# Performance work log

Hardware: AMD Instinct MI355X
Metric: run time of the kernel (lower is better)

The kernel has to match this reference:

```python
import jax, jax.numpy as jnp
import numpy as np

B, N, K, D = 4, 2048, 32, 256
TOKEN_DIM = 256
EGO_DIM = 256
NUM_HEADS = 4
LN_EPS = 1e-6


def masked_softmax(logits, mask, axis):
    mask = mask.astype(jnp.bool_)
    while mask.ndim < logits.ndim:
        mask = mask[..., None]
    neg_big = jnp.finfo(logits.dtype).min
    has_any = jnp.any(mask, axis=axis, keepdims=True)
    masked_logits = jnp.where(mask, logits, neg_big)
    masked_logits = jnp.where(has_any, masked_logits, 0.0)
    weights = jax.nn.softmax(masked_logits, axis=axis)
    weights = jnp.where(mask, weights, 0.0)
    denom = jnp.sum(weights, axis=axis, keepdims=True)
    weights = jnp.where(denom > 0, weights / denom, 0.0)
    return weights


def setup_inputs() -> dict:
    key = jax.random.key(0)
    ks = jax.random.split(key, 10)
    inv_tok = jax.random.normal(ks[0], (B, N, K, D), dtype=jnp.float32)
    ego_ctx = jax.random.normal(ks[1], (B, N, EGO_DIM), dtype=jnp.float32)
    r = jax.random.normal(ks[2], (B, N, K, 3), dtype=jnp.float32)
    u = jax.random.normal(ks[3], (B, N, K, 3), dtype=jnp.float32)
    mask = jax.random.randint(ks[4], (B, N, K), 0, 2).astype(jnp.bool_)
    # params
    W_ego = jax.random.normal(ks[5], (EGO_DIM, TOKEN_DIM), dtype=jnp.float32) * 0.05
    b_ego = jnp.zeros((TOKEN_DIM,), dtype=jnp.float32)
    ln_scale = jnp.ones((D,), dtype=jnp.float32)
    ln_bias = jnp.zeros((D,), dtype=jnp.float32)
    W_h = jax.random.normal(ks[6], (D + TOKEN_DIM, TOKEN_DIM), dtype=jnp.float32) * 0.05
    b_h = jnp.zeros((TOKEN_DIM,), dtype=jnp.float32)
    W_logit = jax.random.normal(ks[7], (TOKEN_DIM, NUM_HEADS), dtype=jnp.float32) * 0.01
    b_logit = jnp.zeros((NUM_HEADS,), dtype=jnp.float32)
    return {"inv_tok": inv_tok, "ego_ctx": ego_ctx, "r": r, "u": u, "mask": mask,
            "W_ego": W_ego, "b_ego": b_ego, "ln_scale": ln_scale, "ln_bias": ln_bias,
            "W_h": W_h, "b_h": b_h, "W_logit": W_logit, "b_logit": b_logit}


def reference(inv_tok, ego_ctx, r, u, mask, W_ego, b_ego, ln_scale, ln_bias, W_h, b_h, W_logit, b_logit):
    # ego context projection, broadcast over K
    ego_h = ego_ctx @ W_ego + b_ego                      # (B,N,T)
    ego_b = jnp.broadcast_to(ego_h[:, :, None, :], (B, N, K, TOKEN_DIM))
    # LayerNorm over last axis of inv_tok
    mean = jnp.mean(inv_tok, axis=-1, keepdims=True)
    var = jnp.var(inv_tok, axis=-1, keepdims=True)
    ln = (inv_tok - mean) * jax.lax.rsqrt(var + LN_EPS) * ln_scale + ln_bias
    h = jnp.concatenate([ln, ego_b], axis=-1)            # (B,N,K,D+T)
    h = jax.nn.gelu(h @ W_h + b_h, approximate=True)     # (B,N,K,T)
    logits = h @ W_logit + b_logit                       # (B,N,K,H)
    alpha = masked_softmax(logits, mask, axis=-2)        # (B,N,K,H)
    v_r = jnp.einsum('bnkh,bnkd->bnhd', alpha, r).reshape(B, N, 3 * NUM_HEADS)
    v_u = jnp.einsum('bnkh,bnkd->bnhd', alpha, u).reshape(B, N, 3 * NUM_HEADS)
    return (v_r, v_u, alpha)
```

## Files before the change

kernel.cpp:

```cpp
#include <hip/hip_runtime.h>

typedef float f32x4 __attribute__((ext_vector_type(4)));
typedef short bf16x8 __attribute__((ext_vector_type(8)));

__device__ __forceinline__ unsigned short f2bf(float f){
    unsigned int u = __builtin_bit_cast(unsigned int, f);
    u = u + 0x7fffu + ((u >> 16) & 1u);
    return (unsigned short)(u >> 16);
}
__device__ __forceinline__ float bf2f(unsigned short h){
    unsigned int u = ((unsigned int)h) << 16;
    return __builtin_bit_cast(float, u);
}
__device__ __forceinline__ unsigned int pk2(float a, float b){
    return (unsigned int)f2bf(a) | ((unsigned int)f2bf(b) << 16);
}
__device__ __forceinline__ float gelu_f(float x){
    float t = x * x;
    float u = fmaf(0.044715f, t, 1.0f);
    float y = 1.5957691216057308f * x * u;
    float e = __expf(-y);
    return x * __builtin_amdgcn_rcpf(1.0f + e);
}

__device__ __forceinline__ int packpos(int k, int n, int NT){
    int kt = k >> 5, quad = (k >> 3) & 3, j = k & 7;
    int nt = n >> 4, nl = n & 15;
    return ((kt * NT + nt) * 64 + quad * 16 + nl) * 8 + j;
}

__global__ __launch_bounds__(256) void prep(const float* __restrict__ Wh,
        const float* __restrict__ Wlogit, const float* __restrict__ Wego,
        const float* __restrict__ b_ego, const float* __restrict__ b_h,
        const float* __restrict__ ln_s, const float* __restrict__ ln_b,
        unsigned short* __restrict__ Bp1, unsigned short* __restrict__ BpL,
        unsigned short* __restrict__ Bpc, float* __restrict__ b_combo,
        float* __restrict__ v1){
    __shared__ float rowbuf[256];
    int bid = blockIdx.x, tid = threadIdx.x;
    if (bid < 64){
        int base = (bid * 256 + tid) * 4;
        int k = base >> 8;
        float sc = ln_s[k];
        for (int e = base; e < base + 4; ++e){
            int n = e & 255;
            Bp1[packpos(k, n, 16)] = f2bf(sc * Wh[k * 256 + n]);
        }
    } else if (bid == 64){
        for (int e = tid * 16; e < tid * 16 + 16; ++e){
            int k = e >> 4, n = e & 15;
            float v = (n < 4) ? Wlogit[k * 4 + n] : 0.0f;
            BpL[packpos(k, n, 1)] = f2bf(v);
        }
    } else if (bid == 65){
        float acc = b_h[tid];
        for (int j = 0; j < 256; ++j) acc += b_ego[j] * Wh[(256 + j) * 256 + tid];
        for (int k = 0; k < 256; ++k) acc += ln_b[k] * Wh[k * 256 + tid];
        b_combo[tid] = acc;
    } else if (bid == 66){
        float acc = 0.f;
        for (int k = 0; k < 256; ++k)
            acc += bf2f(f2bf(ln_s[k] * Wh[k * 256 + tid]));
        v1[tid] = acc;
    } else {
        int k = bid - 67;
        rowbuf[tid] = Wego[k * 256 + tid];
        __syncthreads();
        float acc = 0.f;
        const float4* row4 = (const float4*)rowbuf;
        for (int j4 = 0; j4 < 64; ++j4){
            float4 e = row4[j4];
            int j = j4 * 4;
            acc += e.x * Wh[(256 + j) * 256 + tid];
            acc += e.y * Wh[(257 + j) * 256 + tid];
            acc += e.z * Wh[(258 + j) * 256 + tid];
            acc += e.w * Wh[(259 + j) * 256 + tid];
        }
        Bpc[packpos(k, tid, 16)] = f2bf(acc);
    }
}

__global__ __launch_bounds__(256) void ego_gemm(const float* __restrict__ ego_ctx,
        const unsigned short* __restrict__ Bpc, const float* __restrict__ b_combo,
        unsigned short* __restrict__ ego_term){
    const int tid = threadIdx.x, w = tid >> 6, l = tid & 63;
    const int m0 = blockIdx.x * 16;
    const int row = m0 + (l & 15);
    const int kq = (l >> 4) << 3;
    f32x4 acc[4];
    #pragma unroll
    for (int j = 0; j < 4; ++j) acc[j] = 0;
    #pragma unroll
    for (int kt = 0; kt < 8; ++kt){
        const float* ap = ego_ctx + row * 256 + kt * 32 + kq;
        float4 x0 = *(const float4*)ap;
        float4 x1 = *(const float4*)(ap + 4);
        uint4 pu = {pk2(x0.x, x0.y), pk2(x0.z, x0.w), pk2(x1.x, x1.y), pk2(x1.z, x1.w)};
        bf16x8 a = __builtin_bit_cast(bf16x8, pu);
        #pragma unroll
        for (int j = 0; j < 4; ++j){
            int nt = w * 4 + j;
            bf16x8 b = *(const bf16x8*)&Bpc[((kt * 16 + nt) * 64 + l) * 8];
            acc[j] = __builtin_amdgcn_mfma_f32_16x16x32_bf16(a, b, acc[j], 0, 0, 0);
        }
    }
    const int rq = (l >> 4) << 2, colc = l & 15;
    #pragma unroll
    for (int j = 0; j < 4; ++j){
        int n = (w * 4 + j) * 16 + colc;
        float bc = b_combo[n];
        #pragma unroll
        for (int rg = 0; rg < 4; ++rg)
            ego_term[(m0 + rq + rg) * 256 + n] = f2bf(acc[j][rg] + bc);
    }
}

__global__ __launch_bounds__(256) void main_fused(const float* __restrict__ inv,
        const float* __restrict__ rin, const float* __restrict__ uin,
        const int* __restrict__ mask, const float* __restrict__ b_logit,
        const unsigned short* __restrict__ Bp1, const unsigned short* __restrict__ BpL,
        const unsigned short* __restrict__ ego_term, const float* __restrict__ v1g,
        float* __restrict__ out){

    __shared__ unsigned short Albs[64 * 264];
    __shared__ float2 stats_s[64];
    __shared__ float logit_s[256];
    __shared__ float alpha_s[256];

    const int tid = threadIdx.x;
    const int w = tid >> 6, l = tid & 63;
    const int T0 = blockIdx.x * 64;
    const int bn0 = blockIdx.x * 2;
    const int col = l & 15;
    const int kq = (l >> 4) << 3;

    {
        const int r0 = w * 16;
        const float* base = inv + (T0 + r0) * 256 + l * 4;
        #pragma unroll
        for (int rr = 0; rr < 16; ++rr){
            float4 c = *(const float4*)(base + rr * 256);
            uint2 p;
            p.x = pk2(c.x, c.y);
            p.y = pk2(c.z, c.w);
            *(uint2*)&Albs[(r0 + rr) * 264 + l * 4] = p;
        }
    }
    float v1r[4], egv[2][4];
    #pragma unroll
    for (int i = 0; i < 4; ++i){
        int n = w * 64 + i * 16 + col;
        v1r[i]    = v1g[n];
        egv[0][i] = bf2f(ego_term[(bn0    ) * 256 + n]);
        egv[1][i] = bf2f(ego_term[(bn0 + 1) * 256 + n]);
    }
    __syncthreads();

    f32x4 acc[4][4];
    #pragma unroll
    for (int a = 0; a < 4; ++a)
        #pragma unroll
        for (int b = 0; b < 4; ++b) acc[a][b] = 0;
    f32x4 gacc = 0, sacc = 0;
    bf16x8 ones;
    #pragma unroll
    for (int j = 0; j < 8; ++j) ones[j] = (short)0x3F80;

    #pragma unroll
    for (int kt = 0; kt < 8; ++kt){
        const int ko = kt * 32 + kq;
        bf16x8 af[4], bv[4];
        #pragma unroll
        for (int mt = 0; mt < 4; ++mt)
            af[mt] = *(const bf16x8*)&Albs[(mt * 16 + col) * 264 + ko];
        #pragma unroll
        for (int i = 0; i < 4; ++i)
            bv[i] = *(const bf16x8*)&Bp1[((kt * 16 + (w * 4 + i)) * 64 + l) * 8];
        #pragma unroll
        for (int mt = 0; mt < 4; ++mt){
            if (mt == w){
                gacc = __builtin_amdgcn_mfma_f32_16x16x32_bf16(af[mt], af[mt], gacc, 0, 0, 0);
                sacc = __builtin_amdgcn_mfma_f32_16x16x32_bf16(af[mt], ones,   sacc, 0, 0, 0);
            }
            #pragma unroll
            for (int i = 0; i < 4; ++i)
                acc[mt][i] = __builtin_amdgcn_mfma_f32_16x16x32_bf16(af[mt], bv[i], acc[mt][i], 0, 0, 0);
        }
    }
    if ((col >> 2) == (l >> 4)){
        int rg = col & 3;
        float mean = sacc[rg] * (1.0f / 256.0f);
        float var  = gacc[rg] * (1.0f / 256.0f) - mean * mean;
        float rstd = rsqrtf(var + 1e-6f);
        stats_s[w * 16 + col] = float2{rstd, rstd * mean};
    }
    __syncthreads();

    {
        const int rq = (l >> 4) << 2;
        #pragma unroll
        for (int mt = 0; mt < 4; ++mt){
            const int g = mt >> 1;
            float2 st[4];
            #pragma unroll
            for (int rg = 0; rg < 4; ++rg) st[rg] = stats_s[mt * 16 + rq + rg];
            #pragma unroll
            for (int i = 0; i < 4; ++i){
                const int n = w * 64 + i * 16 + col;
                const float base_t = egv[g][i];
                #pragma unroll
                for (int rg = 0; rg < 4; ++rg){
                    float x = fmaf(st[rg].x, acc[mt][i][rg],
                                   fmaf(-st[rg].y, v1r[i], base_t));
                    Albs[(mt * 16 + rq + rg) * 264 + n] = f2bf(gelu_f(x));
                }
            }
        }
    }
    __syncthreads();

    {
        f32x4 lacc = 0;
        #pragma unroll
        for (int kt = 0; kt < 8; ++kt){
            bf16x8 a = *(const bf16x8*)&Albs[(w * 16 + col) * 264 + kt * 32 + kq];
            bf16x8 b = *(const bf16x8*)&BpL[(kt * 64 + l) * 8];
            lacc = __builtin_amdgcn_mfma_f32_16x16x32_bf16(a, b, lacc, 0, 0, 0);
        }
        if (col < 4){
            float bl = b_logit[col];
            const int rq = (l >> 4) << 2;
            #pragma unroll
            for (int rg = 0; rg < 4; ++rg)
                logit_s[(w * 16 + rq + rg) * 4 + col] = lacc[rg] + bl;
        }
    }
    __syncthreads();

    {
        int g = w >> 1;
        int h = ((w & 1) << 1) + (l >> 5);
        int k = l & 31;
        int valid = mask[T0 + g * 32 + k] != 0;
        float lg = logit_s[(g * 32 + k) * 4 + h];
        float val = valid ? lg : -3.0e38f;
        float mx = val;
        #pragma unroll
        for (int off = 16; off >= 1; off >>= 1)
            mx = fmaxf(mx, __shfl_xor(mx, off));
        float e = valid ? __expf(lg - mx) : 0.0f;
        float ssum = e;
        #pragma unroll
        for (int off = 16; off >= 1; off >>= 1)
            ssum += __shfl_xor(ssum, off);
        float a = (ssum > 0.f) ? e / ssum : 0.0f;
        alpha_s[(g * 32 + k) * 4 + h] = a;
        out[196608 + (T0 + g * 32 + k) * 4 + h] = a;
    }
    __syncthreads();

    if (tid < 48){
        int g = tid / 24, rem = tid % 24;
        int which = rem / 12, hd = rem % 12;
        int h = hd / 3, d = hd % 3;
        const float* src = which ? uin : rin;
        const float* sp = src + (T0 + g * 32) * 3 + d;
        float acc2 = 0.f;
        #pragma unroll
        for (int k = 0; k < 32; ++k)
            acc2 += alpha_s[(g * 32 + k) * 4 + h] * sp[k * 3];
        out[which * 98304 + (bn0 + g) * 12 + hd] = acc2;
    }
}

extern "C" void kernel_launch(void* const* d_in, const int* in_sizes, int n_in,
                              void* d_out, int out_size, void* d_ws, size_t ws_size,
                              hipStream_t stream){
    const float* inv    = (const float*)d_in[0];
    const float* ego    = (const float*)d_in[1];
    const float* rin    = (const float*)d_in[2];
    const float* uin    = (const float*)d_in[3];
    const int*   mask   = (const int*)  d_in[4];
    const float* Wego   = (const float*)d_in[5];
    const float* b_ego  = (const float*)d_in[6];
    const float* ln_s   = (const float*)d_in[7];
    const float* ln_b   = (const float*)d_in[8];
    const float* Wh     = (const float*)d_in[9];
    const float* b_h    = (const float*)d_in[10];
    const float* Wlogit = (const float*)d_in[11];
    const float* b_lg   = (const float*)d_in[12];
    float* out = (float*)d_out;

    unsigned short* wsu = (unsigned short*)d_ws;
    unsigned short* Bp1 = wsu;
    unsigned short* Bpc = wsu + 65536;
    unsigned short* BpL = wsu + 131072;
    float* b_combo      = (float*)(wsu + 135168);
    float* v1           = (float*)(wsu + 135680);
    unsigned short* ego_term = wsu + 136192;

    prep<<<323, 256, 0, stream>>>(Wh, Wlogit, Wego, b_ego, b_h, ln_s, ln_b,
                                  Bp1, BpL, Bpc, b_combo, v1);
    ego_gemm<<<512, 256, 0, stream>>>(ego, Bpc, b_combo, ego_term);
    main_fused<<<4096, 256, 0, stream>>>(inv, rin, uin, mask, b_lg,
                                         Bp1, BpL, ego_term, v1, out);
}
```

Measured before the change: 455.7 us.

## Split main GEMM by rows per wave, drop barriers, fuse softmax reduction

Measured after the change: 506.3 us. 1.11x slower.

```diff
diff --git a/kernel.cpp b/kernel.cpp
--- a/kernel.cpp
+++ b/kernel.cpp
@@ -12,8 +12,13 @@
     unsigned int u = ((unsigned int)h) << 16;
     return __builtin_bit_cast(float, u);
 }
-__device__ __forceinline__ unsigned int pk2(float a, float b){
-    return (unsigned int)f2bf(a) | ((unsigned int)f2bf(b) << 16);
+__device__ __forceinline__ unsigned int pk2_rtz(float a, float b){
+    unsigned int ua = __builtin_bit_cast(unsigned int, a);
+    unsigned int ub = __builtin_bit_cast(unsigned int, b);
+    return (ua >> 16) | (ub & 0xffff0000u);
+}
+__device__ __forceinline__ unsigned short bfrtz(float a){
+    return (unsigned short)(__builtin_bit_cast(unsigned int, a) >> 16);
 }
 __device__ __forceinline__ float gelu_f(float x){
     float t = x * x;
@@ -36,7 +41,7 @@
         unsigned short* __restrict__ Bp1, unsigned short* __restrict__ BpL,
         unsigned short* __restrict__ Bpc, float* __restrict__ b_combo,
         float* __restrict__ v1){
-    __shared__ float rowbuf[256];
+    __shared__ float rowbuf[512];
     int bid = blockIdx.x, tid = threadIdx.x;
     if (bid < 64){
         int base = (bid * 256 + tid) * 4;
@@ -53,14 +58,19 @@
             BpL[packpos(k, n, 1)] = f2bf(v);
         }
     } else if (bid == 65){
+        rowbuf[tid]       = b_ego[tid];
+        rowbuf[256 + tid] = ln_b[tid];
+        __syncthreads();
         float acc = b_h[tid];
-        for (int j = 0; j < 256; ++j) acc += b_ego[j] * Wh[(256 + j) * 256 + tid];
-        for (int k = 0; k < 256; ++k) acc += ln_b[k] * Wh[k * 256 + tid];
+        for (int j = 0; j < 256; ++j) acc += rowbuf[j] * Wh[(256 + j) * 256 + tid];
+        for (int k = 0; k < 256; ++k) acc += rowbuf[256 + k] * Wh[k * 256 + tid];
         b_combo[tid] = acc;
     } else if (bid == 66){
+        rowbuf[tid] = ln_s[tid];
+        __syncthreads();
         float acc = 0.f;
         for (int k = 0; k < 256; ++k)
-            acc += bf2f(f2bf(ln_s[k] * Wh[k * 256 + tid]));
+            acc += bf2f(f2bf(rowbuf[k] * Wh[k * 256 + tid]));
         v1[tid] = acc;
     } else {
         int k = bid - 67;
@@ -95,8 +105,12 @@
         const float* ap = ego_ctx + row * 256 + kt * 32 + kq;
         float4 x0 = *(const float4*)ap;
         float4 x1 = *(const float4*)(ap + 4);
-        uint4 pu = {pk2(x0.x, x0.y), pk2(x0.z, x0.w), pk2(x1.x, x1.y), pk2(x1.z, x1.w)};
-        bf16x8 a = __builtin_bit_cast(bf16x8, pu);
+        unsigned int ua[4];
+        ua[0] = ((unsigned int)f2bf(x0.x)) | ((unsigned int)f2bf(x0.y) << 16);
+        ua[1] = ((unsigned int)f2bf(x0.z)) | ((unsigned int)f2bf(x0.w) << 16);
+        ua[2] = ((unsigned int)f2bf(x1.x)) | ((unsigned int)f2bf(x1.y) << 16);
+        ua[3] = ((unsigned int)f2bf(x1.z)) | ((unsigned int)f2bf(x1.w) << 16);
+        bf16x8 a = __builtin_bit_cast(bf16x8, *(uint4*)ua);
         #pragma unroll
         for (int j = 0; j < 4; ++j){
             int nt = w * 4 + j;
@@ -125,42 +139,40 @@
     __shared__ unsigned short Albs[64 * 264];
     __shared__ float2 stats_s[64];
     __shared__ float logit_s[256];
-    __shared__ float alpha_s[256];
 
     const int tid = threadIdx.x;
     const int w = tid >> 6, l = tid & 63;
     const int T0 = blockIdx.x * 64;
     const int bn0 = blockIdx.x * 2;
-    const int col = l & 15;
-    const int kq = (l >> 4) << 3;
+    const int col = l & 15, quad = l >> 4, kq = quad << 3;
+    const int r0 = w * 16;
+    const int gw = w >> 1;
+
+    const int h_sm = ((w & 1) << 1) + (l >> 5);
+    const int k_sm = l & 31;
+    const int row_sm = gw * 32 + k_sm;
+    const int mvalid = mask[T0 + row_sm];
+    const float blg = b_logit[h_sm];
+    const float* rp = rin + (T0 + row_sm) * 3;
+    const float* up = uin + (T0 + row_sm) * 3;
+    float rv0 = rp[0], rv1 = rp[1], rv2 = rp[2];
+    float uv0 = up[0], uv1 = up[1], uv2 = up[2];
 
     {
-        const int r0 = w * 16;
         const float* base = inv + (T0 + r0) * 256 + l * 4;
         #pragma unroll
         for (int rr = 0; rr < 16; ++rr){
             float4 c = *(const float4*)(base + rr * 256);
             uint2 p;
-            p.x = pk2(c.x, c.y);
-            p.y = pk2(c.z, c.w);
+            p.x = pk2_rtz(c.x, c.y);
+            p.y = pk2_rtz(c.z, c.w);
             *(uint2*)&Albs[(r0 + rr) * 264 + l * 4] = p;
         }
     }
-    float v1r[4], egv[2][4];
-    #pragma unroll
-    for (int i = 0; i < 4; ++i){
-        int n = w * 64 + i * 16 + col;
-        v1r[i]    = v1g[n];
-        egv[0][i] = bf2f(ego_term[(bn0    ) * 256 + n]);
-        egv[1][i] = bf2f(ego_term[(bn0 + 1) * 256 + n]);
-    }
-    __syncthreads();
-
-    f32x4 acc[4][4];
-    #pragma unroll
-    for (int a = 0; a < 4; ++a)
-        #pragma unroll
-        for (int b = 0; b < 4; ++b) acc[a][b] = 0;
+
+    f32x4 acc[16];
+    #pragma unroll
+    for (int i = 0; i < 16; ++i) acc[i] = 0;
     f32x4 gacc = 0, sacc = 0;
     bf16x8 ones;
     #pragma unroll
@@ -168,108 +180,91 @@
 
     #pragma unroll
     for (int kt = 0; kt < 8; ++kt){
-        const int ko = kt * 32 + kq;
-        bf16x8 af[4], bv[4];
-        #pragma unroll
-        for (int mt = 0; mt < 4; ++mt)
-            af[mt] = *(const bf16x8*)&Albs[(mt * 16 + col) * 264 + ko];
-        #pragma unroll
-        for (int i = 0; i < 4; ++i)
-            bv[i] = *(const bf16x8*)&Bp1[((kt * 16 + (w * 4 + i)) * 64 + l) * 8];
-        #pragma unroll
-        for (int mt = 0; mt < 4; ++mt){
-            if (mt == w){
-                gacc = __builtin_amdgcn_mfma_f32_16x16x32_bf16(af[mt], af[mt], gacc, 0, 0, 0);
-                sacc = __builtin_amdgcn_mfma_f32_16x16x32_bf16(af[mt], ones,   sacc, 0, 0, 0);
-            }
-            #pragma unroll
-            for (int i = 0; i < 4; ++i)
-                acc[mt][i] = __builtin_amdgcn_mfma_f32_16x16x32_bf16(af[mt], bv[i], acc[mt][i], 0, 0, 0);
-        }
-    }
-    if ((col >> 2) == (l >> 4)){
+        bf16x8 af = *(const bf16x8*)&Albs[(r0 + col) * 264 + kt * 32 + kq];
+        gacc = __builtin_amdgcn_mfma_f32_16x16x32_bf16(af, af,   gacc, 0, 0, 0);
+        sacc = __builtin_amdgcn_mfma_f32_16x16x32_bf16(af, ones, sacc, 0, 0, 0);
+        #pragma unroll
+        for (int nt = 0; nt < 16; ++nt){
+            bf16x8 bv = *(const bf16x8*)&Bp1[((kt * 16 + nt) * 64 + l) * 8];
+            acc[nt] = __builtin_amdgcn_mfma_f32_16x16x32_bf16(af, bv, acc[nt], 0, 0, 0);
+        }
+    }
+
+    if ((col >> 2) == quad){
         int rg = col & 3;
         float mean = sacc[rg] * (1.0f / 256.0f);
         float var  = gacc[rg] * (1.0f / 256.0f) - mean * mean;
         float rstd = rsqrtf(var + 1e-6f);
-        stats_s[w * 16 + col] = float2{rstd, rstd * mean};
-    }
-    __syncthreads();
-
-    {
-        const int rq = (l >> 4) << 2;
-        #pragma unroll
-        for (int mt = 0; mt < 4; ++mt){
-            const int g = mt >> 1;
-            float2 st[4];
-            #pragma unroll
-            for (int rg = 0; rg < 4; ++rg) st[rg] = stats_s[mt * 16 + rq + rg];
-            #pragma unroll
-            for (int i = 0; i < 4; ++i){
-                const int n = w * 64 + i * 16 + col;
-                const float base_t = egv[g][i];
-                #pragma unroll
-                for (int rg = 0; rg < 4; ++rg){
-                    float x = fmaf(st[rg].x, acc[mt][i][rg],
-                                   fmaf(-st[rg].y, v1r[i], base_t));
-                    Albs[(mt * 16 + rq + rg) * 264 + n] = f2bf(gelu_f(x));
-                }
-            }
-        }
-    }
-    __syncthreads();
+        stats_s[r0 + col] = float2{rstd, rstd * mean};
+    }
+    float2 st[4];
+    #pragma unroll
+    for (int rg = 0; rg < 4; ++rg) st[rg] = stats_s[r0 + quad * 4 + rg];
+
+    #pragma unroll
+    for (int nt = 0; nt < 16; ++nt){
+        const int n = nt * 16 + col;
+        const float v1n = v1g[n];
+        const float egn = bf2f(ego_term[(bn0 + gw) * 256 + n]);
+        #pragma unroll
+        for (int rg = 0; rg < 4; ++rg){
+            float x = fmaf(st[rg].x, acc[nt][rg], fmaf(-st[rg].y, v1n, egn));
+            Albs[(r0 + quad * 4 + rg) * 264 + n] = bfrtz(gelu_f(x));
+        }
+    }
 
     {
         f32x4 lacc = 0;
         #pragma unroll
         for (int kt = 0; kt < 8; ++kt){
-            bf16x8 a = *(const bf16x8*)&Albs[(w * 16 + col) * 264 + kt * 32 + kq];
+            bf16x8 a = *(const bf16x8*)&Albs[(r0 + col) * 264 + kt * 32 + kq];
             bf16x8 b = *(const bf16x8*)&BpL[(kt * 64 + l) * 8];
             lacc = __builtin_amdgcn_mfma_f32_16x16x32_bf16(a, b, lacc, 0, 0, 0);
         }
         if (col < 4){
-            float bl = b_logit[col];
-            const int rq = (l >> 4) << 2;
             #pragma unroll
             for (int rg = 0; rg < 4; ++rg)
-                logit_s[(w * 16 + rq + rg) * 4 + col] = lacc[rg] + bl;
-        }
-    }
+                logit_s[(r0 + quad * 4 + rg) * 4 + col] = lacc[rg];
+        }
+    }
+
     __syncthreads();
 
     {
-        int g = w >> 1;
-        int h = ((w & 1) << 1) + (l >> 5);
-        int k = l & 31;
-        int valid = mask[T0 + g * 32 + k] != 0;
-        float lg = logit_s[(g * 32 + k) * 4 + h];
-        float val = valid ? lg : -3.0e38f;
+        float lg = logit_s[row_sm * 4 + h_sm] + blg;
+        float val = mvalid ? lg : -3.0e38f;
         float mx = val;
         #pragma unroll
         for (int off = 16; off >= 1; off >>= 1)
             mx = fmaxf(mx, __shfl_xor(mx, off));
-        float e = valid ? __expf(lg - mx) : 0.0f;
+        float e = mvalid ? __expf(lg - mx) : 0.0f;
         float ssum = e;
         #pragma unroll
         for (int off = 16; off >= 1; off >>= 1)
             ssum += __shfl_xor(ssum, off);
         float a = (ssum > 0.f) ? e / ssum : 0.0f;
-        alpha_s[(g * 32 + k) * 4 + h] = a;
-        out[196608 + (T0 + g * 32 + k) * 4 + h] = a;
-    }
-    __syncthreads();
-
-    if (tid < 48){
-        int g = tid / 24, rem = tid % 24;
-        int which = rem / 12, hd = rem % 12;
-        int h = hd / 3, d = hd % 3;
-        const float* src = which ? uin : rin;
-        const float* sp = src + (T0 + g * 32) * 3 + d;
-        float acc2 = 0.f;
-        #pragma unroll
-        for (int k = 0; k < 32; ++k)
-            acc2 += alpha_s[(g * 32 + k) * 4 + h] * sp[k * 3];
-        out[which * 98304 + (bn0 + g) * 12 + hd] = acc2;
+        out[196608 + (T0 + row_sm) * 4 + h_sm] = a;
+
+        float p0 = a * rv0, p1 = a * rv1, p2 = a * rv2;
+        float p3 = a * uv0, p4 = a * uv1, p5 = a * uv2;
+        #pragma unroll
+        for (int off = 16; off >= 1; off >>= 1){
+            p0 += __shfl_xor(p0, off);
+            p1 += __shfl_xor(p1, off);
+            p2 += __shfl_xor(p2, off);
+            p3 += __shfl_xor(p3, off);
+            p4 += __shfl_xor(p4, off);
+            p5 += __shfl_xor(p5, off);
+        }
+        if (k_sm == 0){
+            int ob = (bn0 + gw) * 12 + h_sm * 3;
+            out[ob    ] = p0;
+            out[ob + 1] = p1;
+            out[ob + 2] = p2;
+            out[98304 + ob    ] = p3;
+            out[98304 + ob + 1] = p4;
+            out[98304 + ob + 2] = p5;
+        }
     }
 }
 
```
